# Optimization experiments

Hardware: AMD Instinct MI355X
Metric: run time of the kernel (lower is better)

Reference implementation:

```python
import jax, jax.numpy as jnp
import numpy as np

NEG_INF = -1e30  # safe stand-in for float('-inf') under softmax


def setup_inputs() -> dict:
    key = jax.random.key(0)
    ks = jax.random.split(key, 5)
    B, T, D = 4, 2048, 1024
    s = 1.0 / np.sqrt(D)
    return {
        "x": jax.random.normal(ks[0], (B, T, D), dtype=jnp.float32),
        "Wk": jax.random.normal(ks[1], (D, D), dtype=jnp.float32) * s,
        "bk": jnp.zeros((D,), dtype=jnp.float32),
        "Wq": jax.random.normal(ks[2], (D, D), dtype=jnp.float32) * s,
        "bq": jnp.zeros((D,), dtype=jnp.float32),
        "Wv": jax.random.normal(ks[3], (D, D), dtype=jnp.float32) * s,
        "bv": jnp.zeros((D,), dtype=jnp.float32),
        "Wp": jax.random.normal(ks[4], (D, D), dtype=jnp.float32) * s,
        "bp": jnp.zeros((D,), dtype=jnp.float32),
    }


def reference(x, Wk, bk, Wq, bq, Wv, bv, Wp, bp):
    B, T, D = x.shape
    nh = 16
    hd = D // nh
    # QKV projections (weights stored as [in, out])
    q = (x @ Wq + bq).reshape(B, T, nh, hd)
    k = (x @ Wk + bk).reshape(B, T, nh, hd)
    v = (x @ Wv + bv).reshape(B, T, nh, hd)
    # raw attention scores [B, nh, T, T] (module applies no 1/sqrt(d) scale)
    scores = jnp.einsum("bthc,bshc->bhts", q, k)
    causal = jnp.triu(jnp.ones((T, T), dtype=bool), k=1)  # mask future positions
    scores = jnp.where(causal, NEG_INF, scores)
    attn = jax.nn.softmax(scores, axis=-1)  # dropout p=0.0 -> identity
    out = jnp.einsum("bhts,bshc->bthc", attn, v).reshape(B, T, D)
    return out @ Wp + bp
```

## Files before the change

kernel.cpp:

```cpp
#include <hip/hip_runtime.h>
#include <hip/hip_bf16.h>
#include <stdint.h>

#define B_ 4
#define T_ 2048
#define D_ 1024
#define M_ (B_*T_)
#define NH_ 16
#define HD_ 64

typedef __attribute__((ext_vector_type(8))) short bf16x8;
typedef __attribute__((ext_vector_type(4))) float f32x4;

#define GLOAD_LDS16(gp, lp)                                                   \
  __builtin_amdgcn_global_load_lds(                                           \
      (const __attribute__((address_space(1))) void*)(gp),                    \
      (__attribute__((address_space(3))) void*)(lp), 16, 0, 0)

__device__ __forceinline__ unsigned short f2bf(float f) {
  union { float f; unsigned u; } x; x.f = f;
  unsigned r = x.u + 0x7FFFu + ((x.u >> 16) & 1u);
  return (unsigned short)(r >> 16);
}

__global__ __launch_bounds__(256) void cvt_x_kernel(const float* __restrict__ x,
                                                    unsigned short* __restrict__ xb) {
  int i = (blockIdx.x * 256 + threadIdx.x) * 8;
  float4 a = *(const float4*)(x + i);
  float4 b = *(const float4*)(x + i + 4);
  ushort4 lo, hi;
  lo.x = f2bf(a.x); lo.y = f2bf(a.y); lo.z = f2bf(a.z); lo.w = f2bf(a.w);
  hi.x = f2bf(b.x); hi.y = f2bf(b.y); hi.z = f2bf(b.z); hi.w = f2bf(b.w);
  *(ushort4*)(xb + i) = lo;
  *(ushort4*)(xb + i + 4) = hi;
}

__global__ __launch_bounds__(256) void transpose_w4_kernel(
    const float* __restrict__ W0, const float* __restrict__ W1,
    const float* __restrict__ W2, const float* __restrict__ W3,
    unsigned short* __restrict__ O0, unsigned short* __restrict__ O1,
    unsigned short* __restrict__ O2, unsigned short* __restrict__ O3) {
  const float* W = (blockIdx.y == 0) ? W0 : (blockIdx.y == 1) ? W1 : (blockIdx.y == 2) ? W2 : W3;
  unsigned short* Wt = (blockIdx.y == 0) ? O0 : (blockIdx.y == 1) ? O1 : (blockIdx.y == 2) ? O2 : O3;
  __shared__ unsigned short tile[64][72];
  const int bk = (blockIdx.x & 15) * 64;
  const int bn = (blockIdx.x >> 4) * 64;
  const int t = threadIdx.x;
  const int r0 = t >> 4;
  const int c0 = (t & 15) * 4;
#pragma unroll
  for (int p = 0; p < 4; ++p) {
    int r = p * 16 + r0;
    float4 v = *(const float4*)&W[(size_t)(bk + r) * D_ + bn + c0];
    tile[r][c0 + 0] = f2bf(v.x);
    tile[r][c0 + 1] = f2bf(v.y);
    tile[r][c0 + 2] = f2bf(v.z);
    tile[r][c0 + 3] = f2bf(v.w);
  }
  __syncthreads();
#pragma unroll
  for (int p = 0; p < 4; ++p) {
    int n = p * 16 + r0;
    ushort4 o;
    o.x = tile[c0 + 0][n];
    o.y = tile[c0 + 1][n];
    o.z = tile[c0 + 2][n];
    o.w = tile[c0 + 3][n];
    *(ushort4*)&Wt[(size_t)(bn + n) * D_ + bk + c0] = o;
  }
}

__global__ __launch_bounds__(256) void transpose_v_kernel(
    const unsigned short* __restrict__ Vb, unsigned short* __restrict__ Vtg) {
  __shared__ unsigned short tile[64][72];
  const int ct = blockIdx.x * 64;
  const int tt = blockIdx.y * 64;
  const size_t bofs_in  = (size_t)blockIdx.z * T_ * D_;
  const size_t bofs_out = (size_t)blockIdx.z * D_ * T_;
  const int t = threadIdx.x;
  const int r0 = t >> 4;
  const int c0 = (t & 15) * 4;
#pragma unroll
  for (int p = 0; p < 4; ++p) {
    int r = p * 16 + r0;
    *(ushort4*)&tile[r][c0] = *(const ushort4*)&Vb[bofs_in + (size_t)(tt + r) * D_ + ct + c0];
  }
  __syncthreads();
#pragma unroll
  for (int p = 0; p < 4; ++p) {
    int n = p * 16 + r0;
    ushort4 o;
    o.x = tile[c0 + 0][n];
    o.y = tile[c0 + 1][n];
    o.z = tile[c0 + 2][n];
    o.w = tile[c0 + 3][n];
    *(ushort4*)&Vtg[bofs_out + (size_t)(ct + n) * T_ + tt + c0] = o;
  }
}

#define BM 128
#define BN 128
#define BK 64
template <typename OutT>
__device__ __forceinline__ void gemm_core(
    const unsigned short* __restrict__ A, const unsigned short* __restrict__ Bt,
    const float* __restrict__ bias, OutT* __restrict__ C,
    unsigned short* As, unsigned short* Bs, int bm, int bn) {
  const int K = D_, N = D_;
  const int t = threadIdx.x;
  const int lane = t & 63;
  const int w = t >> 6;
  const int wr = (w >> 1) * 64;
  const int wc = (w & 1) * 64;
  const int lr = lane & 15;
  const int lk = (lane >> 4) * 8;
  const int cr = (lane >> 4) * 4;
  const int cc = lane & 15;
  const int srow = lane >> 3;
  const int scol = (lane & 7) * 8;

  f32x4 acc[4][4] = {};

  for (int k0 = 0; k0 < K; k0 += BK) {
#pragma unroll
    for (int i = 0; i < 4; ++i) {
      const int rbase = w * 32 + i * 8;
      GLOAD_LDS16(&A[(size_t)(bm + rbase + srow) * K + k0 + scol], &As[rbase * BK]);
      GLOAD_LDS16(&Bt[(size_t)(bn + rbase + srow) * K + k0 + scol], &Bs[rbase * BK]);
    }
    __syncthreads();
#pragma unroll
    for (int kk = 0; kk < BK; kk += 32) {
      bf16x8 a[4], b[4];
#pragma unroll
      for (int m = 0; m < 4; ++m) a[m] = *(const bf16x8*)&As[(wr + m * 16 + lr) * BK + kk + lk];
#pragma unroll
      for (int n = 0; n < 4; ++n) b[n] = *(const bf16x8*)&Bs[(wc + n * 16 + lr) * BK + kk + lk];
#pragma unroll
      for (int m = 0; m < 4; ++m)
#pragma unroll
        for (int n = 0; n < 4; ++n)
          acc[m][n] = __builtin_amdgcn_mfma_f32_16x16x32_bf16(a[m], b[n], acc[m][n], 0, 0, 0);
    }
    __syncthreads();
  }

#pragma unroll
  for (int m = 0; m < 4; ++m)
#pragma unroll
    for (int n = 0; n < 4; ++n) {
      int col = bn + wc + n * 16 + cc;
      float bv = bias[col];
#pragma unroll
      for (int j = 0; j < 4; ++j) {
        int row = bm + wr + m * 16 + cr + j;
        float v = acc[m][n][j] + bv;
        if constexpr (__is_same(OutT, float)) {
          C[(size_t)row * N + col] = v;
        } else {
          C[(size_t)row * N + col] = f2bf(v);
        }
      }
    }
}

__global__ __launch_bounds__(256) void gemm_qkv_kernel(
    const unsigned short* __restrict__ xb,
    const unsigned short* __restrict__ WqT, const unsigned short* __restrict__ WkT,
    const unsigned short* __restrict__ WvT,
    const float* __restrict__ bq, const float* __restrict__ bk, const float* __restrict__ bv,
    unsigned short* __restrict__ Qb, unsigned short* __restrict__ Kb,
    unsigned short* __restrict__ Vb) {
  __shared__ unsigned short As[BM * BK];
  __shared__ unsigned short Bs[BN * BK];
  const int z = blockIdx.z;
  const unsigned short* Bt = (z == 0) ? WqT : (z == 1) ? WkT : WvT;
  const float* bias = (z == 0) ? bq : (z == 1) ? bk : bv;
  unsigned short* C = (z == 0) ? Qb : (z == 1) ? Kb : Vb;
  gemm_core<unsigned short>(xb, Bt, bias, C, As, Bs, blockIdx.y * BM, blockIdx.x * BN);
}

__global__ __launch_bounds__(256) void gemm_proj_kernel(
    const unsigned short* __restrict__ A, const unsigned short* __restrict__ Bt,
    const float* __restrict__ bias, float* __restrict__ C) {
  __shared__ unsigned short As[BM * BK];
  __shared__ unsigned short Bs[BN * BK];
  gemm_core<float>(A, Bt, bias, C, As, Bs, blockIdx.y * BM, blockIdx.x * BN);
}

__global__ __launch_bounds__(256) void attn_kernel(
    const unsigned short* __restrict__ Qb,
    const unsigned short* __restrict__ Kb,
    const unsigned short* __restrict__ Vtg,
    unsigned short* __restrict__ Ob)
{
  __shared__ unsigned short Ks[64][72];
  __shared__ unsigned short Vt[64][72];
  __shared__ unsigned int   Ps32[4][32][36];

  const int pid = blockIdx.x;
  const int bh = blockIdx.y;
  const int b = bh >> 4, h = bh & 15;
  const int t = threadIdx.x;
  const int lane = t & 63;
  const int w = t >> 6;
  const int lr = lane & 15;
  const int g = lane >> 4;
  const int lk = g * 8;
  const int cr = g * 4;
  const int cc = lane & 15;

  const size_t base   = (size_t)(b * T_) * D_ + h * HD_;
  const size_t vbase  = ((size_t)b * D_ + h * HD_) * T_;

  for (int hp = 0; hp < 2; ++hp) {
    const int qtile = (hp == 0 ? pid : 15 - pid) * 128;

    bf16x8 qf[2][2];
#pragma unroll
    for (int m = 0; m < 2; ++m)
#pragma unroll
      for (int kk = 0; kk < 2; ++kk)
        qf[m][kk] = *(const bf16x8*)&Qb[base + (size_t)(qtile + w * 32 + m * 16 + lr) * D_ + kk * 32 + lk];

    f32x4 acc_o[2][4] = {};
    float mrun[2], lrun[2];
#pragma unroll
    for (int m = 0; m < 2; ++m) { mrun[m] = -1e30f; lrun[m] = 0.f; }

    const int kvend = qtile + 128;
    for (int kvb = 0; kvb < kvend; kvb += 64) {
      __syncthreads();
      {
        int r = t >> 2;
        int c = (t & 3) * 16;
        const unsigned short* kg = &Kb[base + (size_t)(kvb + r) * D_ + c];
        *(int4*)&Ks[r][c]     = *(const int4*)kg;
        *(int4*)&Ks[r][c + 8] = *(const int4*)(kg + 8);
        const unsigned short* vg = &Vtg[vbase + (size_t)r * T_ + kvb + c];
        *(int4*)&Vt[r][c]     = *(const int4*)vg;
        *(int4*)&Vt[r][c + 8] = *(const int4*)(vg + 8);
      }
      __syncthreads();

      f32x4 s[2][4] = {};
#pragma unroll
      for (int kk = 0; kk < 2; ++kk) {
        bf16x8 kf[4];
#pragma unroll
        for (int n = 0; n < 4; ++n) kf[n] = *(const bf16x8*)&Ks[n * 16 + lr][kk * 32 + lk];
#pragma unroll
        for (int m = 0; m < 2; ++m)
#pragma unroll
          for (int n = 0; n < 4; ++n)
            s[m][n] = __builtin_amdgcn_mfma_f32_16x16x32_bf16(kf[n], qf[m][kk], s[m][n], 0, 0, 0);
      }

      const bool diag = (kvb + 64 > qtile);
      bool mact[2];
#pragma unroll
      for (int m = 0; m < 2; ++m) {
        mact[m] = (qtile + w * 32 + m * 16 + 15 >= kvb);
        if (!mact[m]) continue;

        const int qi = qtile + w * 32 + m * 16 + lr;
        if (diag) {
#pragma unroll
          for (int n = 0; n < 4; ++n)
#pragma unroll
            for (int j = 0; j < 4; ++j) {
              int ki = kvb + n * 16 + cr + j;
              if (ki > qi) s[m][n][j] = -1e30f;
            }
        }
        float tmax = -1e30f;
#pragma unroll
        for (int n = 0; n < 4; ++n)
          tmax = fmaxf(tmax, fmaxf(fmaxf(s[m][n][0], s[m][n][1]), fmaxf(s[m][n][2], s[m][n][3])));
        tmax = fmaxf(tmax, __shfl_xor(tmax, 16));
        tmax = fmaxf(tmax, __shfl_xor(tmax, 32));
        float mnew = fmaxf(mrun[m], tmax);
        float sc = __expf(mrun[m] - mnew);
        float psum = 0.f;
#pragma unroll
        for (int n = 0; n < 4; ++n)
#pragma unroll
          for (int j = 0; j < 4; ++j) {
            float p = __expf(s[m][n][j] - mnew);
            s[m][n][j] = p;
            psum += p;
          }
        psum += __shfl_xor(psum, 16);
        psum += __shfl_xor(psum, 32);
        lrun[m] = lrun[m] * sc + psum;
        mrun[m] = mnew;

#pragma unroll
        for (int n = 0; n < 4; ++n)
#pragma unroll
          for (int hh = 0; hh < 2; ++hh) {
            float lo = s[m][n][2 * hh], hi = s[m][n][2 * hh + 1];
            unsigned pk;
            asm("v_cvt_pk_bf16_f32 %0, %1, %2" : "=v"(pk) : "v"(lo), "v"(hi));
            Ps32[w][m * 16 + lr][n * 8 + g * 2 + hh] = pk;
          }

#pragma unroll
        for (int j = 0; j < 4; ++j) {
          float scj = __shfl(sc, (lane & 48) | (cr + j));
#pragma unroll
          for (int n = 0; n < 4; ++n) acc_o[m][n][j] *= scj;
        }
      }

#pragma unroll
      for (int kk = 0; kk < 2; ++kk) {
        bf16x8 vf[4];
#pragma unroll
        for (int n = 0; n < 4; ++n) vf[n] = *(const bf16x8*)&Vt[n * 16 + lr][kk * 32 + lk];
#pragma unroll
        for (int m = 0; m < 2; ++m) {
          if (!mact[m]) continue;
          bf16x8 pa = *(const bf16x8*)((const unsigned short*)&Ps32[w][m * 16 + lr][0] + kk * 32 + lk);
#pragma unroll
          for (int n = 0; n < 4; ++n)
            acc_o[m][n] = __builtin_amdgcn_mfma_f32_16x16x32_bf16(pa, vf[n], acc_o[m][n], 0, 0, 0);
        }
      }
    }

#pragma unroll
    for (int m = 0; m < 2; ++m)
#pragma unroll
      for (int j = 0; j < 4; ++j) {
        float inv = 1.0f / __shfl(lrun[m], (lane & 48) | (cr + j));
#pragma unroll
        for (int n = 0; n < 4; ++n)
          Ob[base + (size_t)(qtile + w * 32 + m * 16 + cr + j) * D_ + n * 16 + cc] =
              f2bf(acc_o[m][n][j] * inv);
      }
  }
}

extern "C" void kernel_launch(void* const* d_in, const int* in_sizes, int n_in,
                              void* d_out, int out_size, void* d_ws, size_t ws_size,
                              hipStream_t stream) {
  const float* x  = (const float*)d_in[0];
  const float* Wk = (const float*)d_in[1];
  const float* bk = (const float*)d_in[2];
  const float* Wq = (const float*)d_in[3];
  const float* bq = (const float*)d_in[4];
  const float* Wv = (const float*)d_in[5];
  const float* bv = (const float*)d_in[6];
  const float* Wp = (const float*)d_in[7];
  const float* bp = (const float*)d_in[8];

  char* ws = (char*)d_ws;
  unsigned short* xb  = (unsigned short*)(ws);
  unsigned short* Ob  = (unsigned short*)(ws);
  unsigned short* WqT = (unsigned short*)(ws + (16ull << 20));
  unsigned short* WkT = (unsigned short*)(ws + (18ull << 20));
  unsigned short* WvT = (unsigned short*)(ws + (20ull << 20));
  unsigned short* WpT = (unsigned short*)(ws + (22ull << 20));
  unsigned short* Qb  = (unsigned short*)(ws + (24ull << 20));
  unsigned short* Kb  = (unsigned short*)(ws + (40ull << 20));
  unsigned short* Vb  = (unsigned short*)(ws + (56ull << 20));
  unsigned short* Vtg = (unsigned short*)(ws + (72ull << 20));

  hipLaunchKernelGGL(cvt_x_kernel, dim3((M_ * D_) / (256 * 8)), dim3(256), 0, stream, x, xb);
  hipLaunchKernelGGL(transpose_w4_kernel, dim3(256, 4), dim3(256), 0, stream,
                     Wq, Wk, Wv, Wp, WqT, WkT, WvT, WpT);

  hipLaunchKernelGGL(gemm_qkv_kernel, dim3(D_ / BN, M_ / BM, 3), dim3(256), 0, stream,
                     xb, WqT, WkT, WvT, bq, bk, bv, Qb, Kb, Vb);

  hipLaunchKernelGGL(transpose_v_kernel, dim3(16, 32, 4), dim3(256), 0, stream, Vb, Vtg);

  hipLaunchKernelGGL(attn_kernel, dim3(8, B_ * NH_), dim3(256), 0, stream, Qb, Kb, Vtg, Ob);

  hipLaunchKernelGGL(gemm_proj_kernel, dim3(D_ / BN, M_ / BM), dim3(256), 0, stream,
                     Ob, WpT, bp, (float*)d_out);
}
```

Baseline: 318.6 us.

## Restructure attention to per-wave 16-row tiles with direct global K/V loads

The attention kernel moves to 512-thread blocks where each of 8 waves owns 16 query rows. K and V^T fragments are now read straight from global memory instead of being staged in shared LDS tiles, which drops the __syncthreads barriers, and each wave stops at its own causal kv bound. It also adds a lazy online-softmax rescale that skips the accumulator rescale unless the running max rises by more than 8. Block index remapping is added to the QKV/proj GEMMs and to attention to group blocks for cache locality. The cost is redundant global/L2 traffic, since all 8 waves fetch the same K/V tiles without LDS sharing.

```diff
diff --git a/kernel.cpp b/kernel.cpp
--- a/kernel.cpp
+++ b/kernel.cpp
@@ -177,7 +177,9 @@
   const unsigned short* Bt = (z == 0) ? WqT : (z == 1) ? WkT : WvT;
   const float* bias = (z == 0) ? bq : (z == 1) ? bk : bv;
   unsigned short* C = (z == 0) ? Qb : (z == 1) ? Kb : Vb;
-  gemm_core<unsigned short>(xb, Bt, bias, C, As, Bs, blockIdx.y * BM, blockIdx.x * BN);
+  const int by = blockIdx.x * 8 + (blockIdx.y & 7);
+  const int bx = blockIdx.y >> 3;
+  gemm_core<unsigned short>(xb, Bt, bias, C, As, Bs, by * BM, bx * BN);
 }
 
 __global__ __launch_bounds__(256) void gemm_proj_kernel(
@@ -185,21 +187,21 @@
     const float* __restrict__ bias, float* __restrict__ C) {
   __shared__ unsigned short As[BM * BK];
   __shared__ unsigned short Bs[BN * BK];
-  gemm_core<float>(A, Bt, bias, C, As, Bs, blockIdx.y * BM, blockIdx.x * BN);
-}
-
-__global__ __launch_bounds__(256) void attn_kernel(
+  const int by = blockIdx.x * 8 + (blockIdx.y & 7);
+  const int bx = blockIdx.y >> 3;
+  gemm_core<float>(A, Bt, bias, C, As, Bs, by * BM, bx * BN);
+}
+
+__global__ __launch_bounds__(512) void attn_kernel(
     const unsigned short* __restrict__ Qb,
     const unsigned short* __restrict__ Kb,
     const unsigned short* __restrict__ Vtg,
     unsigned short* __restrict__ Ob)
 {
-  __shared__ unsigned short Ks[64][72];
-  __shared__ unsigned short Vt[64][72];
-  __shared__ unsigned int   Ps32[4][32][36];
-
-  const int pid = blockIdx.x;
-  const int bh = blockIdx.y;
+  __shared__ unsigned int Ps32[8][16][36];
+
+  const int bh = blockIdx.x * 8 + (blockIdx.y & 7);
+  const int pid = blockIdx.y >> 3;
   const int b = bh >> 4, h = bh & 15;
   const int t = threadIdx.x;
   const int lane = t & 63;
@@ -210,135 +212,105 @@
   const int cr = g * 4;
   const int cc = lane & 15;
 
-  const size_t base   = (size_t)(b * T_) * D_ + h * HD_;
-  const size_t vbase  = ((size_t)b * D_ + h * HD_) * T_;
+  const size_t base  = (size_t)(b * T_) * D_ + h * HD_;
+  const size_t vbase = ((size_t)b * D_ + h * HD_) * T_;
 
   for (int hp = 0; hp < 2; ++hp) {
     const int qtile = (hp == 0 ? pid : 15 - pid) * 128;
-
-    bf16x8 qf[2][2];
-#pragma unroll
-    for (int m = 0; m < 2; ++m)
-#pragma unroll
-      for (int kk = 0; kk < 2; ++kk)
-        qf[m][kk] = *(const bf16x8*)&Qb[base + (size_t)(qtile + w * 32 + m * 16 + lr) * D_ + kk * 32 + lk];
-
-    f32x4 acc_o[2][4] = {};
-    float mrun[2], lrun[2];
-#pragma unroll
-    for (int m = 0; m < 2; ++m) { mrun[m] = -1e30f; lrun[m] = 0.f; }
-
-    const int kvend = qtile + 128;
-    for (int kvb = 0; kvb < kvend; kvb += 64) {
-      __syncthreads();
-      {
-        int r = t >> 2;
-        int c = (t & 3) * 16;
-        const unsigned short* kg = &Kb[base + (size_t)(kvb + r) * D_ + c];
-        *(int4*)&Ks[r][c]     = *(const int4*)kg;
-        *(int4*)&Ks[r][c + 8] = *(const int4*)(kg + 8);
-        const unsigned short* vg = &Vtg[vbase + (size_t)r * T_ + kvb + c];
-        *(int4*)&Vt[r][c]     = *(const int4*)vg;
-        *(int4*)&Vt[r][c + 8] = *(const int4*)(vg + 8);
-      }
-      __syncthreads();
-
-      f32x4 s[2][4] = {};
+    const int qrow0 = qtile + w * 16;
+
+    bf16x8 qf[2];
+#pragma unroll
+    for (int kk = 0; kk < 2; ++kk)
+      qf[kk] = *(const bf16x8*)&Qb[base + (size_t)(qrow0 + lr) * D_ + kk * 32 + lk];
+
+    f32x4 acc_o[4] = {};
+    float mrun = -1e30f, lrun = 0.f;
+
+    const int kvend_w = qtile + ((w >> 2) + 1) * 64;
+    for (int kvb = 0; kvb < kvend_w; kvb += 64) {
+      f32x4 s[4] = {};
 #pragma unroll
       for (int kk = 0; kk < 2; ++kk) {
-        bf16x8 kf[4];
-#pragma unroll
-        for (int n = 0; n < 4; ++n) kf[n] = *(const bf16x8*)&Ks[n * 16 + lr][kk * 32 + lk];
-#pragma unroll
-        for (int m = 0; m < 2; ++m)
-#pragma unroll
-          for (int n = 0; n < 4; ++n)
-            s[m][n] = __builtin_amdgcn_mfma_f32_16x16x32_bf16(kf[n], qf[m][kk], s[m][n], 0, 0, 0);
-      }
-
-      const bool diag = (kvb + 64 > qtile);
-      bool mact[2];
-#pragma unroll
-      for (int m = 0; m < 2; ++m) {
-        mact[m] = (qtile + w * 32 + m * 16 + 15 >= kvb);
-        if (!mact[m]) continue;
-
-        const int qi = qtile + w * 32 + m * 16 + lr;
-        if (diag) {
-#pragma unroll
-          for (int n = 0; n < 4; ++n)
-#pragma unroll
-            for (int j = 0; j < 4; ++j) {
-              int ki = kvb + n * 16 + cr + j;
-              if (ki > qi) s[m][n][j] = -1e30f;
-            }
-        }
-        float tmax = -1e30f;
+#pragma unroll
+        for (int n = 0; n < 4; ++n) {
+          bf16x8 kf = *(const bf16x8*)&Kb[base + (size_t)(kvb + n * 16 + lr) * D_ + kk * 32 + lk];
+          s[n] = __builtin_amdgcn_mfma_f32_16x16x32_bf16(kf, qf[kk], s[n], 0, 0, 0);
+        }
+      }
+
+      const int qi = qrow0 + lr;
+      if (kvb + 63 > qrow0) {
 #pragma unroll
         for (int n = 0; n < 4; ++n)
-          tmax = fmaxf(tmax, fmaxf(fmaxf(s[m][n][0], s[m][n][1]), fmaxf(s[m][n][2], s[m][n][3])));
-        tmax = fmaxf(tmax, __shfl_xor(tmax, 16));
-        tmax = fmaxf(tmax, __shfl_xor(tmax, 32));
-        float mnew = fmaxf(mrun[m], tmax);
-        float sc = __expf(mrun[m] - mnew);
-        float psum = 0.f;
-#pragma unroll
-        for (int n = 0; n < 4; ++n)
 #pragma unroll
           for (int j = 0; j < 4; ++j) {
-            float p = __expf(s[m][n][j] - mnew);
-            s[m][n][j] = p;
-            psum += p;
+            int ki = kvb + n * 16 + cr + j;
+            if (ki > qi) s[n][j] = -1e30f;
           }
-        psum += __shfl_xor(psum, 16);
-        psum += __shfl_xor(psum, 32);
-        lrun[m] = lrun[m] * sc + psum;
-        mrun[m] = mnew;
-
-#pragma unroll
-        for (int n = 0; n < 4; ++n)
-#pragma unroll
-          for (int hh = 0; hh < 2; ++hh) {
-            float lo = s[m][n][2 * hh], hi = s[m][n][2 * hh + 1];
-            unsigned pk;
-            asm("v_cvt_pk_bf16_f32 %0, %1, %2" : "=v"(pk) : "v"(lo), "v"(hi));
-            Ps32[w][m * 16 + lr][n * 8 + g * 2 + hh] = pk;
-          }
-
+      }
+
+      float tmax = -1e30f;
+#pragma unroll
+      for (int n = 0; n < 4; ++n)
+        tmax = fmaxf(tmax, fmaxf(fmaxf(s[n][0], s[n][1]), fmaxf(s[n][2], s[n][3])));
+      tmax = fmaxf(tmax, __shfl_xor(tmax, 16));
+      tmax = fmaxf(tmax, __shfl_xor(tmax, 32));
+
+      float sc = 1.f;
+      if (!__all(tmax <= mrun + 8.f)) {
+        float mnew = fmaxf(mrun, tmax);
+        sc = __expf(mrun - mnew);
+        mrun = mnew;
 #pragma unroll
         for (int j = 0; j < 4; ++j) {
           float scj = __shfl(sc, (lane & 48) | (cr + j));
 #pragma unroll
-          for (int n = 0; n < 4; ++n) acc_o[m][n][j] *= scj;
-        }
-      }
+          for (int n = 0; n < 4; ++n) acc_o[n][j] *= scj;
+        }
+      }
+
+      float psum = 0.f;
+#pragma unroll
+      for (int n = 0; n < 4; ++n)
+#pragma unroll
+        for (int j = 0; j < 4; ++j) {
+          float p = __expf(s[n][j] - mrun);
+          s[n][j] = p;
+          psum += p;
+        }
+      psum += __shfl_xor(psum, 16);
+      psum += __shfl_xor(psum, 32);
+      lrun = lrun * sc + psum;
+
+#pragma unroll
+      for (int n = 0; n < 4; ++n)
+#pragma unroll
+        for (int hh = 0; hh < 2; ++hh) {
+          float lo = s[n][2 * hh], hi = s[n][2 * hh + 1];
+          unsigned pk;
+          asm("v_cvt_pk_bf16_f32 %0, %1, %2" : "=v"(pk) : "v"(lo), "v"(hi));
+          Ps32[w][lr][n * 8 + g * 2 + hh] = pk;
+        }
 
 #pragma unroll
       for (int kk = 0; kk < 2; ++kk) {
-        bf16x8 vf[4];
-#pragma unroll
-        for (int n = 0; n < 4; ++n) vf[n] = *(const bf16x8*)&Vt[n * 16 + lr][kk * 32 + lk];
-#pragma unroll
-        for (int m = 0; m < 2; ++m) {
-          if (!mact[m]) continue;
-          bf16x8 pa = *(const bf16x8*)((const unsigned short*)&Ps32[w][m * 16 + lr][0] + kk * 32 + lk);
-#pragma unroll
-          for (int n = 0; n < 4; ++n)
-            acc_o[m][n] = __builtin_amdgcn_mfma_f32_16x16x32_bf16(pa, vf[n], acc_o[m][n], 0, 0, 0);
-        }
-      }
-    }
-
-#pragma unroll
-    for (int m = 0; m < 2; ++m)
-#pragma unroll
-      for (int j = 0; j < 4; ++j) {
-        float inv = 1.0f / __shfl(lrun[m], (lane & 48) | (cr + j));
-#pragma unroll
-        for (int n = 0; n < 4; ++n)
-          Ob[base + (size_t)(qtile + w * 32 + m * 16 + cr + j) * D_ + n * 16 + cc] =
-              f2bf(acc_o[m][n][j] * inv);
-      }
+        bf16x8 pa = *(const bf16x8*)((const unsigned short*)&Ps32[w][lr][0] + kk * 32 + lk);
+#pragma unroll
+        for (int n = 0; n < 4; ++n) {
+          bf16x8 vf = *(const bf16x8*)&Vtg[vbase + (size_t)(n * 16 + lr) * T_ + kvb + kk * 32 + lk];
+          acc_o[n] = __builtin_amdgcn_mfma_f32_16x16x32_bf16(pa, vf, acc_o[n], 0, 0, 0);
+        }
+      }
+    }
+
+#pragma unroll
+    for (int j = 0; j < 4; ++j) {
+      float inv = 1.0f / __shfl(lrun, (lane & 48) | (cr + j));
+#pragma unroll
+      for (int n = 0; n < 4; ++n)
+        Ob[base + (size_t)(qrow0 + cr + j) * D_ + n * 16 + cc] = f2bf(acc_o[n][j] * inv);
+    }
   }
 }
 
@@ -376,7 +348,7 @@
 
   hipLaunchKernelGGL(transpose_v_kernel, dim3(16, 32, 4), dim3(256), 0, stream, Vb, Vtg);
 
-  hipLaunchKernelGGL(attn_kernel, dim3(8, B_ * NH_), dim3(256), 0, stream, Qb, Kb, Vtg, Ob);
+  hipLaunchKernelGGL(attn_kernel, dim3(8, 64), dim3(512), 0, stream, Qb, Kb, Vtg, Ob);
 
   hipLaunchKernelGGL(gemm_proj_kernel, dim3(D_ / BN, M_ / BM), dim3(256), 0, stream,
                      Ob, WpT, bp, (float*)d_out);
```

Result: slower. 451.2 us (+41.6%).
